# Kernel tuning notes

Hardware: AMD Instinct MI355X
Metric: run time of the kernel (lower is better)

The kernel has to match this reference:

```python
import jax, jax.numpy as jnp
import numpy as np

H, K, D = 24, 2, 128          # query heads, kv heads, head_size
HIDDEN = H * D                # 3072
ROPE_THETA = 10000.0


def setup_inputs() -> dict:
    key = jax.random.key(0)
    ks = jax.random.split(key, 6)
    B, S = 2, 2048
    T = B * S
    hidden_states = jax.random.normal(ks[0], (T, HIDDEN), dtype=jnp.float32)
    w_qkv = jax.random.normal(ks[1], ((H + 2 * K) * D, HIDDEN), dtype=jnp.float32) * (HIDDEN ** -0.5)
    b_qkv = jax.random.normal(ks[2], ((H + 2 * K) * D,), dtype=jnp.float32) * 0.02
    w_o = jax.random.normal(ks[3], (HIDDEN, H * D), dtype=jnp.float32) * (HIDDEN ** -0.5)
    b_o = jax.random.normal(ks[4], (HIDDEN,), dtype=jnp.float32) * 0.02
    # rotary tables: positions restart per sequence (flash-varlen prefill layout)
    pos = jnp.tile(jnp.arange(S, dtype=jnp.float32), B)            # [T]
    inv_freq = 1.0 / (ROPE_THETA ** (jnp.arange(0, D, 2, dtype=jnp.float32) / D))  # [D/2]
    freqs = pos[:, None] * inv_freq[None, :]                        # [T, D/2]
    return {
        "hidden_states": hidden_states,
        "w_qkv": w_qkv, "b_qkv": b_qkv,
        "w_o": w_o, "b_o": b_o,
        "cos": jnp.cos(freqs), "sin": jnp.sin(freqs),
        "seq_len": S, "window": 1024,
    }


def _rope(x, cos, sin):
    # rotate-half (neox) style, as in TGI PositionRotaryEmbedding
    half = x.shape[-1] // 2
    x1, x2 = x[..., :half], x[..., half:]
    c, s = cos[:, None, :], sin[:, None, :]   # broadcast over head dim
    return jnp.concatenate([x1 * c - x2 * s, x2 * c + x1 * s], axis=-1)


def reference(hidden_states, w_qkv, b_qkv, w_o, b_o, cos, sin, seq_len, window):
    T = hidden_states.shape[0]
    B = T // seq_len
    scale = D ** -0.5

    # fused QKV projection
    qkv = hidden_states @ w_qkv.T + b_qkv                 # [T, (H+2K)*D]
    q = qkv[:, : H * D].reshape(T, H, D)
    kv = qkv[:, H * D:].reshape(T, 2, K, D)
    k, v = kv[:, 0], kv[:, 1]                             # [T, K, D]

    q = _rope(q, cos, sin)
    k = _rope(k, cos, sin)

    # GQA: expand kv heads to query heads
    groups = H // K
    qb = q.reshape(B, seq_len, H, D)
    kb = jnp.repeat(k.reshape(B, seq_len, K, D), groups, axis=2)  # [B,S,H,D]
    vb = jnp.repeat(v.reshape(B, seq_len, K, D), groups, axis=2)

    scores = jnp.einsum("bqhd,bkhd->bhqk", qb, kb) * scale        # [B,H,S,S]
    idx = jnp.arange(seq_len)
    delta = idx[:, None] - idx[None, :]
    mask = (delta >= 0) & (delta < window)                        # causal + sliding window
    scores = jnp.where(mask[None, None], scores, jnp.float32(-1e9))
    attn = jax.nn.softmax(scores, axis=-1)
    out = jnp.einsum("bhqk,bkhd->bqhd", attn, vb).reshape(T, H * D)
    return out @ w_o.T + b_o
```

## Files before the change

kernel.cpp:

```cpp
#include <hip/hip_runtime.h>
#include <hip/hip_bf16.h>

typedef __attribute__((ext_vector_type(8))) short bf16x8;
typedef __attribute__((ext_vector_type(4))) float f32x4;

__device__ __forceinline__ short f2bf_bits(float f) {
    __hip_bfloat16 h = __float2bfloat16(f);
    short s;
    __builtin_memcpy(&s, &h, 2);
    return s;
}

__device__ __forceinline__ float bf_bits2f(short s) {
    unsigned int u = ((unsigned int)(unsigned short)s) << 16;
    float f;
    __builtin_memcpy(&f, &u, 4);
    return f;
}

__device__ __forceinline__ bf16x8 load8(const float* p) {
    float4 a = *(const float4*)p;
    float4 b = *(const float4*)(p + 4);
    bf16x8 r;
    r[0] = f2bf_bits(a.x); r[1] = f2bf_bits(a.y);
    r[2] = f2bf_bits(a.z); r[3] = f2bf_bits(a.w);
    r[4] = f2bf_bits(b.x); r[5] = f2bf_bits(b.y);
    r[6] = f2bf_bits(b.z); r[7] = f2bf_bits(b.w);
    return r;
}
__device__ __forceinline__ bf16x8 load8(const __hip_bfloat16* p) {
    return *(const bf16x8*)p;
}

__device__ __forceinline__ void store_out(__hip_bfloat16* p, float v) {
    *p = __float2bfloat16(v);
}
__device__ __forceinline__ void store_out(float* p, float v) { *p = v; }

__global__ void cvt3_f32_bf16(const float* __restrict__ a, short* __restrict__ da, int na8,
                              const float* __restrict__ b, short* __restrict__ db, int nb8,
                              const float* __restrict__ c, short* __restrict__ dc, int nc8) {
    int i = blockIdx.x * 256 + threadIdx.x;
    if (i < na8) {
        *(bf16x8*)(da + (size_t)i * 8) = load8(a + (size_t)i * 8);
    } else if ((i -= na8) < nb8) {
        *(bf16x8*)(db + (size_t)i * 8) = load8(b + (size_t)i * 8);
    } else if ((i -= nb8) < nc8) {
        *(bf16x8*)(dc + (size_t)i * 8) = load8(c + (size_t)i * 8);
    }
}

#define GB_REG 65536

__device__ __forceinline__ int half_off(int buf, int half) {
    return buf * 32768 + half * 16384;
}

template <typename TC>
__global__ __launch_bounds__(512) void gemm256(
    const __hip_bfloat16* __restrict__ A, const __hip_bfloat16* __restrict__ B,
    const float* __restrict__ bias, TC* __restrict__ C, int M, int N, int K)
{
    __shared__ char smem[131072];

    const int tid  = threadIdx.x;
    const int lane = tid & 63;
    const int wid  = tid >> 6;
    const int quad = lane >> 4;
    const int m16  = lane & 15;
    const int wmg  = wid >> 2;
    const int wng  = wid & 3;
    const int bhalf = wng >> 1;
    const int bsub  = (wng & 1) * 4;

    const int gx  = gridDim.x;
    const int nwg = gx * gridDim.y;
    int lin = blockIdx.y * gx + blockIdx.x;
    if ((nwg & 7) == 0) {
        int q = nwg >> 3;
        lin = (lin & 7) * q + (lin >> 3);
    }
    const int bn = lin % gx, bm = lin / gx;
    const int mBase = bm * 256, nBase = bn * 256;

    const int roff = (m16 << 6) | ((quad * 16) ^ (((m16 >> 1) & 3) << 4));

    int r_s[2], c_s[2];
    #pragma unroll
    for (int l = 0; l < 2; ++l) {
        int sub = l * 8 + wid;
        int r16 = (tid >> 2) & 15;
        int cb  = ((tid & 3) * 16) ^ (((r16 >> 1) & 3) << 4);
        r_s[l] = (sub >> 1) * 16 + r16;
        c_s[l] = (sub & 1) * 32 + (cb >> 1);
    }

    const __hip_bfloat16* Ab = A + (size_t)mBase * K;
    const __hip_bfloat16* Bb = B + (size_t)nBase * K;

    auto stage = [&](int region, const __hip_bfloat16* base, int buf, int half, int tile) {
        const __hip_bfloat16* gb = base + (size_t)(half * 128) * K + tile * 64;
        #pragma unroll
        for (int l = 0; l < 2; ++l) {
            const __hip_bfloat16* g = gb + (size_t)r_s[l] * K + c_s[l];
            short* lb = (short*)(smem + region + half_off(buf, half) + l * 8192 + wid * 1024);
            __builtin_amdgcn_global_load_lds(
                (__attribute__((address_space(1))) void*)g,
                (__attribute__((address_space(3))) void*)lb, 16, 0, 0);
        }
    };

    f32x4 acc[8][4] = {};
    bf16x8 afr[4][2];
    bf16x8 bfr[2][2][2];

    auto LD_A = [&](int buf, int g) {
        const char* base = smem + half_off(buf, wmg) + (g ? 8192 : 0);
        #pragma unroll
        for (int m = 0; m < 4; ++m)
            #pragma unroll
            for (int ks = 0; ks < 2; ++ks)
                afr[m][ks] = *(const bf16x8*)(base + ((m * 2 + ks) << 10) + roff);
    };
    auto LD_B = [&](int buf, int g) {
        const char* base = smem + GB_REG + half_off(buf, bhalf) + ((bsub + g * 2) << 11);
        #pragma unroll
        for (int j = 0; j < 2; ++j)
            #pragma unroll
            for (int ks = 0; ks < 2; ++ks)
                bfr[g][j][ks] = *(const bf16x8*)(base + ((j * 2 + ks) << 10) + roff);
    };
    auto MM = [&](int mo, int g) {
        #pragma unroll
        for (int m = 0; m < 4; ++m)
            #pragma unroll
            for (int j = 0; j < 2; ++j)
                #pragma unroll
                for (int ks = 0; ks < 2; ++ks)
                    acc[mo + m][g * 2 + j] = __builtin_amdgcn_mfma_f32_16x16x32_bf16(
                        afr[m][ks], bfr[g][j][ks], acc[mo + m][g * 2 + j], 0, 0, 0);
    };

#define SBAR() __builtin_amdgcn_s_barrier()
#define WAIT_LGKM0() do { asm volatile("s_waitcnt lgkmcnt(0)" ::: "memory"); \
                          __builtin_amdgcn_sched_barrier(0); } while (0)
#define WAIT_VM4()   do { asm volatile("s_waitcnt vmcnt(4)"   ::: "memory"); \
                          __builtin_amdgcn_sched_barrier(0); } while (0)

    const int NT = K >> 6;

    stage(GB_REG, Bb, 0, 0, 0);
    stage(0,      Ab, 0, 0, 0);
    stage(GB_REG, Bb, 0, 1, 0);
    stage(0,      Ab, 0, 1, 0);
    stage(GB_REG, Bb, 1, 0, 1);
    stage(0,      Ab, 1, 0, 1);
    WAIT_VM4();
    SBAR();

    for (int i = 0; i < (NT >> 1); ++i) {
        const int to = 2 * i + 1;
        const int t2 = min(2 * i + 2, NT - 1);
        const int t3 = min(2 * i + 3, NT - 1);
        LD_A(0, 0); LD_B(0, 0);
        stage(GB_REG, Bb, 1, 1, to);
        SBAR(); WAIT_LGKM0();
        __builtin_amdgcn_s_setprio(1); MM(0, 0); __builtin_amdgcn_s_setprio(0);
        SBAR();
        LD_B(0, 1);
        stage(0, Ab, 1, 1, to);
        SBAR(); WAIT_LGKM0();
        __builtin_amdgcn_s_setprio(1); MM(0, 1); __builtin_amdgcn_s_setprio(0);
        SBAR();
        LD_A(0, 1);
        stage(GB_REG, Bb, 0, 0, t2);
        SBAR(); WAIT_LGKM0();
        __builtin_amdgcn_s_setprio(1); MM(4, 1); __builtin_amdgcn_s_setprio(0);
        SBAR();
        stage(0, Ab, 0, 0, t2);
        WAIT_VM4();
        SBAR();
        __builtin_amdgcn_s_setprio(1); MM(4, 0); __builtin_amdgcn_s_setprio(0);
        SBAR();
        LD_A(1, 0); LD_B(1, 0);
        stage(GB_REG, Bb, 0, 1, t2);
        SBAR(); WAIT_LGKM0();
        __builtin_amdgcn_s_setprio(1); MM(0, 0); __builtin_amdgcn_s_setprio(0);
        SBAR();
        LD_B(1, 1);
        stage(0, Ab, 0, 1, t2);
        SBAR(); WAIT_LGKM0();
        __builtin_amdgcn_s_setprio(1); MM(0, 1); __builtin_amdgcn_s_setprio(0);
        SBAR();
        LD_A(1, 1);
        stage(GB_REG, Bb, 1, 0, t3);
        SBAR(); WAIT_LGKM0();
        __builtin_amdgcn_s_setprio(1); MM(4, 1); __builtin_amdgcn_s_setprio(0);
        SBAR();
        stage(0, Ab, 1, 0, t3);
        WAIT_VM4();
        SBAR();
        __builtin_amdgcn_s_setprio(1); MM(4, 0); __builtin_amdgcn_s_setprio(0);
        SBAR();
    }

#undef SBAR
#undef WAIT_LGKM0
#undef WAIT_VM4

    float bv[4];
    #pragma unroll
    for (int j = 0; j < 4; ++j)
        bv[j] = bias[nBase + wng * 64 + j * 16 + m16];

    #pragma unroll
    for (int mf = 0; mf < 8; ++mf) {
        #pragma unroll
        for (int j = 0; j < 4; ++j) {
            const int col = nBase + wng * 64 + j * 16 + m16;
            #pragma unroll
            for (int r = 0; r < 4; ++r) {
                const int row = mBase + wmg * 128 + mf * 16 + quad * 4 + r;
                store_out(&C[(size_t)row * N + col], acc[mf][j][r] + bv[j]);
            }
        }
    }
}

#define LDSS 40

template <typename TA, typename TB, typename TC>
__global__ __launch_bounds__(256) void gemm_bt_bias(
    const TA* __restrict__ A, const TB* __restrict__ B,
    const float* __restrict__ bias, TC* __restrict__ C, int M, int N, int K)
{
    __shared__ short As[128 * LDSS];
    __shared__ short Bs[128 * LDSS];

    const int tid  = threadIdx.x;
    const int lane = tid & 63;
    const int wid  = tid >> 6;
    const int quad = lane >> 4;
    const int m16  = lane & 15;

    const int mBase = blockIdx.y * 128;
    const int nBase = blockIdx.x * 128;
    const int wm = (wid >> 1) * 64;
    const int wn = (wid & 1) * 64;

    f32x4 acc[4][4] = {};
    const int srow = tid >> 2;
    const int sgrp = (tid & 3) * 8;

    for (int kt = 0; kt < K; kt += 32) {
        __syncthreads();
        for (int p = 0; p < 2; ++p) {
            int r = srow + p * 64;
            *(bf16x8*)(&As[r * LDSS + sgrp]) =
                load8(A + (size_t)(mBase + r) * K + kt + sgrp);
            *(bf16x8*)(&Bs[r * LDSS + sgrp]) =
                load8(B + (size_t)(nBase + r) * K + kt + sgrp);
        }
        __syncthreads();

        bf16x8 afr[4], bfr[4];
        #pragma unroll
        for (int i = 0; i < 4; ++i)
            afr[i] = *(const bf16x8*)(&As[(wm + 16 * i + m16) * LDSS + quad * 8]);
        #pragma unroll
        for (int j = 0; j < 4; ++j)
            bfr[j] = *(const bf16x8*)(&Bs[(wn + 16 * j + m16) * LDSS + quad * 8]);
        #pragma unroll
        for (int i = 0; i < 4; ++i)
            #pragma unroll
            for (int j = 0; j < 4; ++j)
                acc[i][j] = __builtin_amdgcn_mfma_f32_16x16x32_bf16(
                    afr[i], bfr[j], acc[i][j], 0, 0, 0);
    }

    float bv[4];
    #pragma unroll
    for (int j = 0; j < 4; ++j)
        bv[j] = bias[nBase + wn + 16 * j + m16];

    #pragma unroll
    for (int i = 0; i < 4; ++i)
        #pragma unroll
        for (int j = 0; j < 4; ++j) {
            int col = nBase + wn + 16 * j + m16;
            #pragma unroll
            for (int r = 0; r < 4; ++r) {
                int row = mBase + wm + 16 * i + quad * 4 + r;
                store_out(&C[(size_t)row * N + col], acc[i][j][r] + bv[j]);
            }
        }
}

__global__ void rope_kernel(__hip_bfloat16* __restrict__ qkv,
                            const float* __restrict__ cosb,
                            const float* __restrict__ sinb, int T)
{
    int idx = blockIdx.x * 256 + threadIdx.x;
    int total = T * 26 * 8;
    if (idx >= total) return;
    int j = idx & 7;
    int h = (idx >> 3) % 26;
    int t = idx / (26 * 8);
    int col = (h < 24) ? h * 128 : 3072 + (h - 24) * 128;
    int d0 = j * 8;
    size_t base = (size_t)t * 3584 + col + d0;
    bf16x8 x1 = *(const bf16x8*)((const short*)qkv + base);
    bf16x8 x2 = *(const bf16x8*)((const short*)qkv + base + 64);
    float4 c0 = *(const float4*)(cosb + t * 64 + d0);
    float4 c1 = *(const float4*)(cosb + t * 64 + d0 + 4);
    float4 s0 = *(const float4*)(sinb + t * 64 + d0);
    float4 s1 = *(const float4*)(sinb + t * 64 + d0 + 4);
    float cc[8] = {c0.x, c0.y, c0.z, c0.w, c1.x, c1.y, c1.z, c1.w};
    float ss[8] = {s0.x, s0.y, s0.z, s0.w, s1.x, s1.y, s1.z, s1.w};
    bf16x8 o1, o2;
    #pragma unroll
    for (int i = 0; i < 8; ++i) {
        float f1 = bf_bits2f(x1[i]);
        float f2 = bf_bits2f(x2[i]);
        o1[i] = f2bf_bits(f1 * cc[i] - f2 * ss[i]);
        o2[i] = f2bf_bits(f2 * cc[i] + f1 * ss[i]);
    }
    *(bf16x8*)((short*)qkv + base)      = o1;
    *(bf16x8*)((short*)qkv + base + 64) = o2;
}

#define SM_SHIFT 12.0f

__global__ __launch_bounds__(256, 3) void attn_kernel(
    const __hip_bfloat16* __restrict__ qkv,
    __hip_bfloat16* __restrict__ out,
    const int* __restrict__ seq_len_p, const int* __restrict__ window_p)
{
    const int S = seq_len_p[0];
    const int window = window_p[0];
    const float scale = 0.088388347648318447f;

    const int h   = blockIdx.y;
    const int kvh = h / 12;
    const int tid  = threadIdx.x;
    const int lane = tid & 63;
    const int wid  = tid >> 6;
    const int quad = lane >> 4;
    const int m16  = lane & 15;

    const int nbb = S >> 7;
    const int b   = blockIdx.x / nbb;
    const int ib  = blockIdx.x - b * nbb;
    const int qb  = (nbb - 1 - ib) << 7;
    const int qb_global = b * S + qb;

    __shared__ short Vt[128 * 72];
    __shared__ short Ps[4][32 * 40];

    const size_t kvrow0 = (size_t)(b * S) * 3584 + 3072 + kvh * 128;

    bf16x8 qf[2][4];
    {
        const __hip_bfloat16* qp =
            qkv + (size_t)(qb_global + wid * 32 + m16) * 3584 + h * 128;
        #pragma unroll
        for (int qt = 0; qt < 2; ++qt)
            #pragma unroll
            for (int dc = 0; dc < 4; ++dc)
                qf[qt][dc] = *(const bf16x8*)(qp + qt * 16 * 3584 + dc * 32 + quad * 8);
    }

    f32x4 accO[2][8] = {};
    float lqt[2] = {0.f, 0.f};

    int ka0 = qb - window + 1;
    if (ka0 < 0) ka0 = 0;
    ka0 &= ~31;
    const int kend = qb + 128;
    const int niter = (kend - ka0) >> 5;

    const int skey = tid & 31;
    const int sgg0 = tid >> 5;
    const int sgg1 = sgg0 + 8;

    for (int it = 0; it < niter; ++it) {
        const int kt = ka0 + it * 32;

        bf16x8 v0 = *(const bf16x8*)(qkv + kvrow0 + (size_t)(kt + skey) * 3584 + 256 + sgg0 * 8);
        bf16x8 v1 = *(const bf16x8*)(qkv + kvrow0 + (size_t)(kt + skey) * 3584 + 256 + sgg1 * 8);

        __builtin_amdgcn_s_barrier();

        {
            short* dst0 = &Vt[(sgg0 * 8) * 72 + skey + (sgg0 & 1) * 32];
            short* dst1 = &Vt[(sgg1 * 8) * 72 + skey + (sgg1 & 1) * 32];
            #pragma unroll
            for (int i2 = 0; i2 < 8; ++i2) dst0[i2 * 72] = v0[i2];
            #pragma unroll
            for (int i2 = 0; i2 < 8; ++i2) dst1[i2 * 72] = v1[i2];
        }
        asm volatile("s_waitcnt lgkmcnt(0)" ::: "memory");
        __builtin_amdgcn_s_barrier();
        __builtin_amdgcn_sched_barrier(0);

        f32x4 sacc[2][2] = {};
        #pragma unroll
        for (int st = 0; st < 2; ++st) {
            const __hip_bfloat16* kp =
                qkv + kvrow0 + (size_t)(kt + st * 16 + m16) * 3584;
            #pragma unroll
            for (int dc = 0; dc < 4; ++dc) {
                bf16x8 kf = *(const bf16x8*)(kp + dc * 32 + quad * 8);
                sacc[st][0] = __builtin_amdgcn_mfma_f32_16x16x32_bf16(
                    kf, qf[0][dc], sacc[st][0], 0, 0, 0);
                sacc[st][1] = __builtin_amdgcn_mfma_f32_16x16x32_bf16(
                    kf, qf[1][dc], sacc[st][1], 0, 0, 0);
            }
        }

        #pragma unroll
        for (int qt = 0; qt < 2; ++qt) {
            const int qmin = qb + wid * 32 + qt * 16;
            short* prow = &Ps[wid][(qt * 16 + m16) * 40];
            float psum = 0.f;
            if (kt <= qmin - 31 && kt >= qmin + 16 - window) {
                #pragma unroll
                for (int st = 0; st < 2; ++st)
                    #pragma unroll
                    for (int r = 0; r < 4; ++r) {
                        float pp = __expf(fminf(
                            sacc[st][qt][r] * scale - SM_SHIFT, 80.f));
                        psum += pp;
                        prow[st * 16 + quad * 4 + r] = f2bf_bits(pp);
                    }
            } else {
                const int dl_base = (qmin + m16) - (kt + quad * 4);
                #pragma unroll
                for (int st = 0; st < 2; ++st)
                    #pragma unroll
                    for (int r = 0; r < 4; ++r) {
                        int dl = dl_base - st * 16 - r;
                        float pp = ((unsigned)dl < (unsigned)window)
                            ? __expf(fminf(sacc[st][qt][r] * scale - SM_SHIFT, 80.f))
                            : 0.f;
                        psum += pp;
                        prow[st * 16 + quad * 4 + r] = f2bf_bits(pp);
                    }
            }
            psum += __shfl_xor(psum, 16, 64);
            psum += __shfl_xor(psum, 32, 64);
            lqt[qt] += psum;
        }

        bf16x8 pf0 = *(const bf16x8*)(&Ps[wid][(0  + m16) * 40 + quad * 8]);
        bf16x8 pf1 = *(const bf16x8*)(&Ps[wid][(16 + m16) * 40 + quad * 8]);
        __builtin_amdgcn_s_setprio(1);
        #pragma unroll
        for (int dt = 0; dt < 8; ++dt) {
            int row = dt * 16 + m16;
            bf16x8 vf = *(const bf16x8*)(&Vt[row * 72 + quad * 8 + ((row >> 3) & 1) * 32]);
            accO[0][dt] = __builtin_amdgcn_mfma_f32_16x16x32_bf16(pf0, vf, accO[0][dt], 0, 0, 0);
            accO[1][dt] = __builtin_amdgcn_mfma_f32_16x16x32_bf16(pf1, vf, accO[1][dt], 0, 0, 0);
        }
        __builtin_amdgcn_s_setprio(0);
    }

    #pragma unroll
    for (int qt = 0; qt < 2; ++qt) {
        float li[4];
        #pragma unroll
        for (int r = 0; r < 4; ++r)
            li[r] = 1.0f / __shfl(lqt[qt], quad * 4 + r, 64);
        #pragma unroll
        for (int r = 0; r < 4; ++r) {
            int t = qb_global + wid * 32 + qt * 16 + quad * 4 + r;
            __hip_bfloat16* op = out + (size_t)t * 3072 + h * 128 + m16;
            #pragma unroll
            for (int dt = 0; dt < 8; ++dt)
                op[dt * 16] = __float2bfloat16(accO[qt][dt][r] * li[r]);
        }
    }
}

extern "C" void kernel_launch(void* const* d_in, const int* in_sizes, int n_in,
                              void* d_out, int out_size, void* d_ws, size_t ws_size,
                              hipStream_t stream) {
    const float* hidden = (const float*)d_in[0];
    const float* w_qkv  = (const float*)d_in[1];
    const float* b_qkv  = (const float*)d_in[2];
    const float* w_o    = (const float*)d_in[3];
    const float* b_o    = (const float*)d_in[4];
    const float* cosb   = (const float*)d_in[5];
    const float* sinb   = (const float*)d_in[6];
    const int* seq_len_p = (const int*)d_in[7];
    const int* window_p  = (const int*)d_in[8];

    const int HID  = in_sizes[4];
    const int NQKV = in_sizes[2];
    const int T    = in_sizes[0] / HID;

    size_t off = 0;
    auto alloc = [&](size_t bytes) {
        char* p = (char*)d_ws + off;
        off = (off + bytes + 255) & ~(size_t)255;
        return p;
    };
    __hip_bfloat16* qkv      = (__hip_bfloat16*)alloc((size_t)T * NQKV * 2);
    __hip_bfloat16* attn_out = (__hip_bfloat16*)alloc((size_t)T * HID * 2);
    __hip_bfloat16* hid_bf = (__hip_bfloat16*)alloc((size_t)T * HID * 2);
    __hip_bfloat16* wq_bf  = (__hip_bfloat16*)alloc((size_t)NQKV * HID * 2);
    __hip_bfloat16* wo_bf  = (__hip_bfloat16*)alloc((size_t)HID * HID * 2);
    const bool pre = (ws_size >= off);
    const bool big = pre && (T % 256 == 0) && (NQKV % 256 == 0) &&
                     (HID % 256 == 0) && (HID % 64 == 0);

    dim3 blk(256);

    if (big) {
        int n8h = T * HID / 8, n8q = NQKV * HID / 8, n8o = HID * HID / 8;
        int n8 = n8h + n8q + n8o;
        cvt3_f32_bf16<<<dim3((n8 + 255) / 256), blk, 0, stream>>>(
            hidden, (short*)hid_bf, n8h, w_qkv, (short*)wq_bf, n8q,
            w_o, (short*)wo_bf, n8o);
        gemm256<__hip_bfloat16><<<dim3(NQKV / 256, T / 256), dim3(512), 0, stream>>>(
            hid_bf, wq_bf, b_qkv, qkv, T, NQKV, HID);
    } else {
        gemm_bt_bias<float, float, __hip_bfloat16>
            <<<dim3(NQKV / 128, T / 128), blk, 0, stream>>>(
            hidden, w_qkv, b_qkv, qkv, T, NQKV, HID);
    }

    int total = T * 26 * 8;
    rope_kernel<<<dim3((total + 255) / 256), blk, 0, stream>>>(qkv, cosb, sinb, T);

    attn_kernel<<<dim3(T / 128, 24), blk, 0, stream>>>(qkv, attn_out, seq_len_p, window_p);

    if (big) {
        gemm256<float><<<dim3(HID / 256, T / 256), dim3(512), 0, stream>>>(
            attn_out, wo_bf, b_o, (float*)d_out, T, HID, HID);
    } else {
        gemm_bt_bias<__hip_bfloat16, float, float>
            <<<dim3(HID / 128, T / 128), blk, 0, stream>>>(
            attn_out, w_o, b_o, (float*)d_out, T, HID, HID);
    }
}
```

Baseline: 480.7 us.

## Keep P in registers via permuted key order, process 64 keys per iteration

The attention loop now handles 64 keys per iteration, split into two 32-key sub-blocks, with a double-plane transposed V tile in shared memory. K rows are loaded in a permuted order so that each lane's score accumulator already matches the MFMA A-operand layout for P. This removes the per-wave Ps shared-memory round trip and halves the number of barriers. V is packed into dword stores for the transpose. The costs are more registers, a larger V tile in LDS, and a coarser window start (aligned to 64), which adds some masked work.

```diff
diff --git a/kernel.cpp b/kernel.cpp
--- a/kernel.cpp
+++ b/kernel.cpp
@@ -330,6 +330,7 @@
 }
 
 #define SM_SHIFT 12.0f
+#define VPLANE 9248
 
 __global__ __launch_bounds__(256, 3) void attn_kernel(
     const __hip_bfloat16* __restrict__ qkv,
@@ -354,8 +355,7 @@
     const int qb  = (nbb - 1 - ib) << 7;
     const int qb_global = b * S + qb;
 
-    __shared__ short Vt[128 * 72];
-    __shared__ short Ps[4][32 * 40];
+    __shared__ short Vt[2 * VPLANE];
 
     const size_t kvrow0 = (size_t)(b * S) * 3584 + 3072 + kvh * 128;
 
@@ -375,92 +375,116 @@
 
     int ka0 = qb - window + 1;
     if (ka0 < 0) ka0 = 0;
-    ka0 &= ~31;
+    ka0 &= ~63;
     const int kend = qb + 128;
-    const int niter = (kend - ka0) >> 5;
-
-    const int skey = tid & 31;
-    const int sgg0 = tid >> 5;
-    const int sgg1 = sgg0 + 8;
+    const int niter = (kend - ka0) >> 6;
+
+    const int jkey = tid & 31;
+    const int gg0  = tid >> 5;
+    const int phi_base = ((m16 >> 2) << 3) + (m16 & 3);
 
     for (int it = 0; it < niter; ++it) {
-        const int kt = ka0 + it * 32;
-
-        bf16x8 v0 = *(const bf16x8*)(qkv + kvrow0 + (size_t)(kt + skey) * 3584 + 256 + sgg0 * 8);
-        bf16x8 v1 = *(const bf16x8*)(qkv + kvrow0 + (size_t)(kt + skey) * 3584 + 256 + sgg1 * 8);
+        const int kt = ka0 + it * 64;
+
+        const __hip_bfloat16* vp =
+            qkv + kvrow0 + (size_t)(kt + 2 * jkey) * 3584 + 256;
+        bf16x8 va0 = *(const bf16x8*)(vp + gg0 * 8);
+        bf16x8 vb0 = *(const bf16x8*)(vp + 3584 + gg0 * 8);
+        bf16x8 va1 = *(const bf16x8*)(vp + (gg0 + 8) * 8);
+        bf16x8 vb1 = *(const bf16x8*)(vp + 3584 + (gg0 + 8) * 8);
+        __builtin_amdgcn_sched_barrier(0);
 
         __builtin_amdgcn_s_barrier();
 
         {
-            short* dst0 = &Vt[(sgg0 * 8) * 72 + skey + (sgg0 & 1) * 32];
-            short* dst1 = &Vt[(sgg1 * 8) * 72 + skey + (sgg1 & 1) * 32];
-            #pragma unroll
-            for (int i2 = 0; i2 < 8; ++i2) dst0[i2 * 72] = v0[i2];
-            #pragma unroll
-            for (int i2 = 0; i2 < 8; ++i2) dst1[i2 * 72] = v1[i2];
+            short* pl = &Vt[(jkey >> 4) * VPLANE];
+            const int colsh = 2 * (jkey & 15);
+            #pragma unroll
+            for (int i2 = 0; i2 < 8; ++i2) {
+                unsigned dw0 = (unsigned)(unsigned short)va0[i2] |
+                               ((unsigned)(unsigned short)vb0[i2] << 16);
+                *(unsigned*)(pl + (gg0 * 8 + i2) * 72 + colsh + (gg0 & 1) * 32) = dw0;
+            }
+            #pragma unroll
+            for (int i2 = 0; i2 < 8; ++i2) {
+                unsigned dw1 = (unsigned)(unsigned short)va1[i2] |
+                               ((unsigned)(unsigned short)vb1[i2] << 16);
+                *(unsigned*)(pl + ((gg0 + 8) * 8 + i2) * 72 + colsh + ((gg0 + 8) & 1) * 32) = dw1;
+            }
         }
         asm volatile("s_waitcnt lgkmcnt(0)" ::: "memory");
         __builtin_amdgcn_s_barrier();
         __builtin_amdgcn_sched_barrier(0);
 
-        f32x4 sacc[2][2] = {};
-        #pragma unroll
-        for (int st = 0; st < 2; ++st) {
-            const __hip_bfloat16* kp =
-                qkv + kvrow0 + (size_t)(kt + st * 16 + m16) * 3584;
-            #pragma unroll
-            for (int dc = 0; dc < 4; ++dc) {
-                bf16x8 kf = *(const bf16x8*)(kp + dc * 32 + quad * 8);
-                sacc[st][0] = __builtin_amdgcn_mfma_f32_16x16x32_bf16(
-                    kf, qf[0][dc], sacc[st][0], 0, 0, 0);
-                sacc[st][1] = __builtin_amdgcn_mfma_f32_16x16x32_bf16(
-                    kf, qf[1][dc], sacc[st][1], 0, 0, 0);
-            }
-        }
-
-        #pragma unroll
-        for (int qt = 0; qt < 2; ++qt) {
-            const int qmin = qb + wid * 32 + qt * 16;
-            short* prow = &Ps[wid][(qt * 16 + m16) * 40];
-            float psum = 0.f;
-            if (kt <= qmin - 31 && kt >= qmin + 16 - window) {
+        bf16x8 pf[2][2];
+
+        #pragma unroll
+        for (int kb = 0; kb < 2; ++kb) {
+            const int ktb = kt + kb * 32;
+            f32x4 sacc[2][2] = {};
+            #pragma unroll
+            for (int st = 0; st < 2; ++st) {
+                const __hip_bfloat16* kp =
+                    qkv + kvrow0 + (size_t)(ktb + phi_base + st * 4) * 3584 + quad * 8;
                 #pragma unroll
-                for (int st = 0; st < 2; ++st)
+                for (int dc = 0; dc < 4; ++dc) {
+                    bf16x8 kf = *(const bf16x8*)(kp + dc * 32);
+                    sacc[st][0] = __builtin_amdgcn_mfma_f32_16x16x32_bf16(
+                        kf, qf[0][dc], sacc[st][0], 0, 0, 0);
+                    sacc[st][1] = __builtin_amdgcn_mfma_f32_16x16x32_bf16(
+                        kf, qf[1][dc], sacc[st][1], 0, 0, 0);
+                }
+            }
+
+            #pragma unroll
+            for (int qt = 0; qt < 2; ++qt) {
+                const int qmin = qb + wid * 32 + qt * 16;
+                bf16x8 pfv;
+                float psum = 0.f;
+                if (ktb <= qmin - 31 && ktb >= qmin + 16 - window) {
                     #pragma unroll
-                    for (int r = 0; r < 4; ++r) {
-                        float pp = __expf(fminf(
-                            sacc[st][qt][r] * scale - SM_SHIFT, 80.f));
-                        psum += pp;
-                        prow[st * 16 + quad * 4 + r] = f2bf_bits(pp);
-                    }
-            } else {
-                const int dl_base = (qmin + m16) - (kt + quad * 4);
-                #pragma unroll
-                for (int st = 0; st < 2; ++st)
+                    for (int st = 0; st < 2; ++st)
+                        #pragma unroll
+                        for (int r = 0; r < 4; ++r) {
+                            float pp = __expf(fminf(
+                                sacc[st][qt][r] * scale - SM_SHIFT, 80.f));
+                            psum += pp;
+                            pfv[st * 4 + r] = f2bf_bits(pp);
+                        }
+                } else {
+                    const int dl_base = (qmin + m16) - (ktb + quad * 8);
                     #pragma unroll
-                    for (int r = 0; r < 4; ++r) {
-                        int dl = dl_base - st * 16 - r;
-                        float pp = ((unsigned)dl < (unsigned)window)
-                            ? __expf(fminf(sacc[st][qt][r] * scale - SM_SHIFT, 80.f))
-                            : 0.f;
-                        psum += pp;
-                        prow[st * 16 + quad * 4 + r] = f2bf_bits(pp);
-                    }
-            }
-            psum += __shfl_xor(psum, 16, 64);
-            psum += __shfl_xor(psum, 32, 64);
-            lqt[qt] += psum;
-        }
-
-        bf16x8 pf0 = *(const bf16x8*)(&Ps[wid][(0  + m16) * 40 + quad * 8]);
-        bf16x8 pf1 = *(const bf16x8*)(&Ps[wid][(16 + m16) * 40 + quad * 8]);
+                    for (int st = 0; st < 2; ++st)
+                        #pragma unroll
+                        for (int r = 0; r < 4; ++r) {
+                            int dl = dl_base - st * 4 - r;
+                            float pp = ((unsigned)dl < (unsigned)window)
+                                ? __expf(fminf(sacc[st][qt][r] * scale - SM_SHIFT, 80.f))
+                                : 0.f;
+                            psum += pp;
+                            pfv[st * 4 + r] = f2bf_bits(pp);
+                        }
+                }
+                psum += __shfl_xor(psum, 16, 64);
+                psum += __shfl_xor(psum, 32, 64);
+                lqt[qt] += psum;
+                pf[qt][kb] = pfv;
+            }
+        }
+
         __builtin_amdgcn_s_setprio(1);
         #pragma unroll
-        for (int dt = 0; dt < 8; ++dt) {
-            int row = dt * 16 + m16;
-            bf16x8 vf = *(const bf16x8*)(&Vt[row * 72 + quad * 8 + ((row >> 3) & 1) * 32]);
-            accO[0][dt] = __builtin_amdgcn_mfma_f32_16x16x32_bf16(pf0, vf, accO[0][dt], 0, 0, 0);
-            accO[1][dt] = __builtin_amdgcn_mfma_f32_16x16x32_bf16(pf1, vf, accO[1][dt], 0, 0, 0);
+        for (int kb = 0; kb < 2; ++kb) {
+            const short* pl = &Vt[kb * VPLANE];
+            #pragma unroll
+            for (int dt = 0; dt < 8; ++dt) {
+                int row = dt * 16 + m16;
+                bf16x8 vf = *(const bf16x8*)(pl + row * 72 + quad * 8 + ((row >> 3) & 1) * 32);
+                accO[0][dt] = __builtin_amdgcn_mfma_f32_16x16x32_bf16(
+                    pf[0][kb], vf, accO[0][dt], 0, 0, 0);
+                accO[1][dt] = __builtin_amdgcn_mfma_f32_16x16x32_bf16(
+                    pf[1][kb], vf, accO[1][dt], 0, 0, 0);
+            }
         }
         __builtin_amdgcn_s_setprio(0);
     }
```

Result: faster. 470.5 us (-2.1%).
